# Optimization experiments

Measured on AMD Instinct MI355X. Metric: run time of the kernel, lower is better.

## Reference

```python
import jax, jax.numpy as jnp
import numpy as np

E = 800000   # num edges
N = 50000    # num atoms
C = 128      # in_channels
RBF = 20     # rbf_dim
T = 1        # num_target


def setup_inputs() -> dict:
    key = jax.random.key(0)
    ks = jax.random.split(key, 12)
    return {
        "x_scalar": jax.random.normal(ks[0], (E, C), dtype=jnp.float32),
        "rbf": jax.random.normal(ks[1], (E, RBF), dtype=jnp.float32),
        "envelop_para": jax.random.uniform(ks[2], (E, 1), dtype=jnp.float32),
        "edge_index_0": jax.random.randint(ks[3], (E,), 0, N),
        "num_atoms": N,
        # learned parameters (biases initialized to zero per reset_parameters)
        "W_rbf": jax.random.normal(ks[4], (C, RBF), dtype=jnp.float32) * 0.05,
        "b_rbf": jnp.zeros((C,), dtype=jnp.float32),
        "W1": jax.random.normal(ks[5], (C, C), dtype=jnp.float32) * 0.05,
        "b1": jnp.zeros((C,), dtype=jnp.float32),
        "W2": jax.random.normal(ks[6], (C, C), dtype=jnp.float32) * 0.05,
        "b2": jnp.zeros((C,), dtype=jnp.float32),
        "W3": jax.random.normal(ks[7], (T, C), dtype=jnp.float32) * 0.05,
        "b3": jnp.zeros((T,), dtype=jnp.float32),
    }


def reference(x_scalar, rbf, envelop_para, edge_index_0, num_atoms,
              W_rbf, b_rbf, W1, b1, W2, b2, W3, b3):
    # per-edge filter: Linear(rbf) * envelope, then modulate node features
    rbf_filter = (rbf @ W_rbf.T + b_rbf) * envelop_para  # [E, C]
    msg = rbf_filter * x_scalar                           # [E, C]
    # scatter_add over destination atoms
    out = jax.ops.segment_sum(msg, edge_index_0, num_segments=num_atoms)  # [N, C]
    # small MLP head: Linear+SiLU, Linear+SiLU, Linear -> num_target
    out = jax.nn.silu(out @ W1.T + b1)
    out = jax.nn.silu(out @ W2.T + b2)
    out = out @ W3.T + b3                                 # [N, T]
    return out
```

## Files before the change

### kernel.cpp

```cpp
#include <hip/hip_runtime.h>
#include <hip/hip_bf16.h>

#define C 128
#define RBFD 20
#define NATOMS 50000
#define SCAN_CHUNK 1024
#define SLAB 128
#define SS 32
#define NSS (SLAB / SS)

__global__ __launch_bounds__(256) void setup_kernel(
    const float* __restrict__ W1, const float* __restrict__ W2,
    float* __restrict__ W1T, float* __restrict__ W2T,
    int* __restrict__ count, float4* __restrict__ acc4,
    int n, int acc_quads)
{
    const int t = blockIdx.x * blockDim.x + threadIdx.x;
    const int stride = gridDim.x * blockDim.x;
    if (t < C * C) {
        int k = t / C;
        int c = t % C;
        W1T[t] = W1[c * C + k];
        W2T[t] = W2[c * C + k];
    }
    for (int i = t; i < n; i += stride) count[i] = 0;
    const float4 z = make_float4(0.f, 0.f, 0.f, 0.f);
    for (int i = t; i < acc_quads; i += stride) acc4[i] = z;
}

__global__ __launch_bounds__(256) void histogram_kernel(
    const int* __restrict__ idx, int* __restrict__ count, int E)
{
    int e = blockIdx.x * blockDim.x + threadIdx.x;
    if (e < E) atomicAdd(&count[idx[e]], 1);
}

__global__ __launch_bounds__(256) void scan_partials_kernel(
    const int* __restrict__ count, int* __restrict__ partial, int n)
{
    __shared__ int sm[256];
    const int start = blockIdx.x * SCAN_CHUNK;
    int s = 0;
    for (int i = threadIdx.x; i < SCAN_CHUNK; i += 256) {
        int g = start + i;
        if (g < n) s += count[g];
    }
    sm[threadIdx.x] = s;
    __syncthreads();
    for (int off = 128; off > 0; off >>= 1) {
        if (threadIdx.x < off) sm[threadIdx.x] += sm[threadIdx.x + off];
        __syncthreads();
    }
    if (threadIdx.x == 0) partial[blockIdx.x] = sm[0];
}

__global__ void scan_chunkbase_kernel(int* __restrict__ partial,
                                      int* __restrict__ base,
                                      int nchunks, int n)
{
    if (threadIdx.x == 0 && blockIdx.x == 0) {
        int run = 0;
        for (int k = 0; k < nchunks; ++k) {
            int t = partial[k];
            partial[k] = run;
            run += t;
        }
        base[n] = run;
    }
}

__global__ __launch_bounds__(1024) void scan_apply_kernel(
    const int* __restrict__ count, const int* __restrict__ chunk_base,
    int* __restrict__ base, int* __restrict__ cursor, int n)
{
    __shared__ int sm[SCAN_CHUNK];
    const int t = threadIdx.x;
    const int i = blockIdx.x * SCAN_CHUNK + t;
    int v = (i < n) ? count[i] : 0;
    sm[t] = v;
    __syncthreads();
    for (int off = 1; off < SCAN_CHUNK; off <<= 1) {
        int tmp = (t >= off) ? sm[t - off] : 0;
        __syncthreads();
        sm[t] += tmp;
        __syncthreads();
    }
    if (i < n) {
        int excl = sm[t] - v + chunk_base[blockIdx.x];
        base[i] = excl;
        cursor[i] = excl;
    }
}

__global__ __launch_bounds__(256) void fill_perm_kernel(
    const int* __restrict__ idx, int* __restrict__ cursor,
    int* __restrict__ perm, int* __restrict__ own, int E)
{
    int e = blockIdx.x * blockDim.x + threadIdx.x;
    if (e < E) {
        int a = idx[e];
        int pos = atomicAdd(&cursor[a], 1);
        perm[pos] = e;
        own[pos] = a;
    }
}

__global__ __launch_bounds__(128, 2) void gather_kernel(
    const float* __restrict__ x,
    const float* __restrict__ rbf,
    const float* __restrict__ env,
    const int*   __restrict__ perm,
    const int*   __restrict__ own,
    const float* __restrict__ Wrbf,
    const float* __restrict__ brbf,
    float* __restrict__ acc)
{
    __shared__ int   e_s[SLAB];
    __shared__ float env_s[SLAB];
    __shared__ int   own_s[SLAB];
    __shared__ float rbf_s[2][SS][RBFD];

    const int tid = threadIdx.x;
    const int p0  = blockIdx.x * SLAB;

    {
        const int e = perm[p0 + tid];
        e_s[tid]   = e;
        env_s[tid] = env[e];
        own_s[tid] = own[p0 + tid];
    }

    float w[RBFD];
#pragma unroll
    for (int r = 0; r < RBFD; ++r) w[r] = Wrbf[tid * RBFD + r];
    const float bias = brbf[tid];

    __syncthreads();

    const int first_own = own_s[0];
    int   cur_own = first_own;
    float sum = 0.0f;

#define FLUSH()                                                                \
    do {                                                                       \
        if (cur_own == first_own)                                              \
            unsafeAtomicAdd(&acc[(size_t)cur_own * C + tid], sum);             \
        else acc[(size_t)cur_own * C + tid] = sum;                             \
    } while (0)

    float xr[2][SS];
    float st[5];

#pragma unroll
    for (int p = 0; p < 5; ++p) {
        const int g = p * 128 + tid;
        st[p] = rbf[(size_t)e_s[g / RBFD] * RBFD + (g % RBFD)];
    }
#pragma unroll
    for (int i = 0; i < SS; ++i)
        xr[0][i] = x[(size_t)e_s[i] * C + tid];
    __builtin_amdgcn_sched_barrier(0);
#pragma unroll
    for (int p = 0; p < 5; ++p) {
        const int g = p * 128 + tid;
        rbf_s[0][g / RBFD][g % RBFD] = st[p];
    }
    __syncthreads();

#pragma unroll
    for (int ss = 0; ss < NSS; ++ss) {
        const int sbase = ss * SS;
        const int cur   = ss & 1;

        if (ss + 1 < NSS) {
#pragma unroll
            for (int p = 0; p < 5; ++p) {
                const int g = p * 128 + tid;
                st[p] = rbf[(size_t)e_s[sbase + SS + g / RBFD] * RBFD + (g % RBFD)];
            }
#pragma unroll
            for (int i = 0; i < SS; ++i)
                xr[cur ^ 1][i] = x[(size_t)e_s[sbase + SS + i] * C + tid];
        }
        __builtin_amdgcn_sched_barrier(0);

#pragma unroll
        for (int j = 0; j < SS; ++j) {
            const float4* q = reinterpret_cast<const float4*>(&rbf_s[cur][j][0]);
            const float4 a = q[0], b = q[1], c = q[2], d = q[3], e4 = q[4];
            float f = bias;
            f = fmaf(a.x,  w[0],  f); f = fmaf(a.y,  w[1],  f);
            f = fmaf(a.z,  w[2],  f); f = fmaf(a.w,  w[3],  f);
            f = fmaf(b.x,  w[4],  f); f = fmaf(b.y,  w[5],  f);
            f = fmaf(b.z,  w[6],  f); f = fmaf(b.w,  w[7],  f);
            f = fmaf(c.x,  w[8],  f); f = fmaf(c.y,  w[9],  f);
            f = fmaf(c.z,  w[10], f); f = fmaf(c.w,  w[11], f);
            f = fmaf(d.x,  w[12], f); f = fmaf(d.y,  w[13], f);
            f = fmaf(d.z,  w[14], f); f = fmaf(d.w,  w[15], f);
            f = fmaf(e4.x, w[16], f); f = fmaf(e4.y, w[17], f);
            f = fmaf(e4.z, w[18], f); f = fmaf(e4.w, w[19], f);

            const float v = f * env_s[sbase + j] * xr[cur][j];
            const int   o = own_s[sbase + j];
            if (o != cur_own) { FLUSH(); sum = 0.0f; cur_own = o; }
            sum += v;
        }

        if (ss + 1 < NSS) {
#pragma unroll
            for (int p = 0; p < 5; ++p) {
                const int g = p * 128 + tid;
                rbf_s[cur ^ 1][g / RBFD][g % RBFD] = st[p];
            }
        }
        __syncthreads();
    }
    unsafeAtomicAdd(&acc[(size_t)cur_own * C + tid], sum);
#undef FLUSH
}

__device__ __forceinline__ float silu_f(float v) {
    return v * (1.0f / (1.0f + __expf(-v)));
}

__global__ __launch_bounds__(256) void mlp_head_kernel(
    const float* __restrict__ acc,
    const float* __restrict__ W1T,
    const float* __restrict__ b1,
    const float* __restrict__ W2T,
    const float* __restrict__ b2,
    const float* __restrict__ W3,
    const float* __restrict__ b3,
    float* __restrict__ out,
    int natoms)
{
    __shared__ float As[C][C + 1];

    const int tid = threadIdx.x;
    const int a0  = blockIdx.x * C;
    const int tc  = tid & 15;
    const int ta  = tid >> 4;
    const int abase = ta * 8;
    const int cbase = tc * 8;

    {
        const int sub = tid >> 7;
        const int k   = tid & 127;
        for (int pair = 0; pair < 64; ++pair) {
            const int al = pair * 2 + sub;
            const int a  = a0 + al;
            float v = (a < natoms) ? acc[(size_t)a * C + k] : 0.0f;
            As[k][al] = v;
        }
    }
    __syncthreads();

    float r[8][8];

#pragma unroll
    for (int i = 0; i < 8; ++i)
#pragma unroll
        for (int j = 0; j < 8; ++j) r[i][j] = 0.0f;

#pragma unroll 2
    for (int k = 0; k < C; ++k) {
        float4 bq0 = *reinterpret_cast<const float4*>(W1T + k * C + cbase);
        float4 bq1 = *reinterpret_cast<const float4*>(W1T + k * C + cbase + 4);
        float bv[8] = {bq0.x, bq0.y, bq0.z, bq0.w, bq1.x, bq1.y, bq1.z, bq1.w};
        float av[8];
#pragma unroll
        for (int i = 0; i < 8; ++i) av[i] = As[k][abase + i];
#pragma unroll
        for (int i = 0; i < 8; ++i)
#pragma unroll
            for (int j = 0; j < 8; ++j) r[i][j] = fmaf(av[i], bv[j], r[i][j]);
    }

    __syncthreads();
    {
        float bb[8];
#pragma unroll
        for (int j = 0; j < 8; ++j) bb[j] = b1[cbase + j];
#pragma unroll
        for (int i = 0; i < 8; ++i)
#pragma unroll
            for (int j = 0; j < 8; ++j)
                As[cbase + j][abase + i] = silu_f(r[i][j] + bb[j]);
    }
    __syncthreads();

#pragma unroll
    for (int i = 0; i < 8; ++i)
#pragma unroll
        for (int j = 0; j < 8; ++j) r[i][j] = 0.0f;

#pragma unroll 2
    for (int k = 0; k < C; ++k) {
        float4 bq0 = *reinterpret_cast<const float4*>(W2T + k * C + cbase);
        float4 bq1 = *reinterpret_cast<const float4*>(W2T + k * C + cbase + 4);
        float bv[8] = {bq0.x, bq0.y, bq0.z, bq0.w, bq1.x, bq1.y, bq1.z, bq1.w};
        float av[8];
#pragma unroll
        for (int i = 0; i < 8; ++i) av[i] = As[k][abase + i];
#pragma unroll
        for (int i = 0; i < 8; ++i)
#pragma unroll
            for (int j = 0; j < 8; ++j) r[i][j] = fmaf(av[i], bv[j], r[i][j]);
    }

    __syncthreads();

    {
        float bb[8], w3v[8];
#pragma unroll
        for (int j = 0; j < 8; ++j) bb[j] = b2[cbase + j];
        float4 wq0 = *reinterpret_cast<const float4*>(W3 + cbase);
        float4 wq1 = *reinterpret_cast<const float4*>(W3 + cbase + 4);
        w3v[0]=wq0.x; w3v[1]=wq0.y; w3v[2]=wq0.z; w3v[3]=wq0.w;
        w3v[4]=wq1.x; w3v[5]=wq1.y; w3v[6]=wq1.z; w3v[7]=wq1.w;

#pragma unroll
        for (int i = 0; i < 8; ++i) {
            float p = 0.0f;
#pragma unroll
            for (int j = 0; j < 8; ++j)
                p = fmaf(silu_f(r[i][j] + bb[j]), w3v[j], p);
            As[abase + i][tc] = p;
        }
    }
    __syncthreads();

    if (tid < C) {
        const int a = a0 + tid;
        if (a < natoms) {
            float s = 0.0f;
#pragma unroll
            for (int t = 0; t < 16; ++t) s += As[tid][t];
            out[a] = s + b3[0];
        }
    }
}

extern "C" void kernel_launch(void* const* d_in, const int* in_sizes, int n_in,
                              void* d_out, int out_size, void* d_ws, size_t ws_size,
                              hipStream_t stream) {
    const float* x      = (const float*)d_in[0];
    const float* rbf    = (const float*)d_in[1];
    const float* env    = (const float*)d_in[2];
    const int*   idx    = (const int*)  d_in[3];
    const float* Wrbf   = (const float*)d_in[5];
    const float* brbf   = (const float*)d_in[6];
    const float* W1     = (const float*)d_in[7];
    const float* b1     = (const float*)d_in[8];
    const float* W2     = (const float*)d_in[9];
    const float* b2     = (const float*)d_in[10];
    const float* W3     = (const float*)d_in[11];
    const float* b3     = (const float*)d_in[12];
    float*       out    = (float*)d_out;

    const int E = in_sizes[0] / C;
    const int N = NATOMS;
    const int nchunks = (N + SCAN_CHUNK - 1) / SCAN_CHUNK;

    float* acc     = (float*)d_ws;
    float* W1T     = acc + (size_t)N * C;
    float* W2T     = W1T + C * C;
    int*   count   = (int*)(W2T + C * C);
    int*   base    = count + N;
    int*   cursor  = base + (N + 1);
    int*   partial = cursor + N;
    int*   perm    = partial + 64;
    int*   own     = perm + E;

    setup_kernel<<<2048, 256, 0, stream>>>(W1, W2, W1T, W2T, count,
                                           (float4*)acc, N, (N * C) / 4);

    histogram_kernel<<<(E + 255) / 256, 256, 0, stream>>>(idx, count, E);
    scan_partials_kernel<<<nchunks, 256, 0, stream>>>(count, partial, N);
    scan_chunkbase_kernel<<<1, 64, 0, stream>>>(partial, base, nchunks, N);
    scan_apply_kernel<<<nchunks, SCAN_CHUNK, 0, stream>>>(count, partial, base, cursor, N);
    fill_perm_kernel<<<(E + 255) / 256, 256, 0, stream>>>(idx, cursor, perm, own, E);

    gather_kernel<<<E / SLAB, 128, 0, stream>>>(x, rbf, env, perm, own,
                                                Wrbf, brbf, acc);

    const int tiles = (N + C - 1) / C;
    mlp_head_kernel<<<tiles, 256, 0, stream>>>(acc, W1T, b1, W2T, b2, W3, b3, out, N);
}
```

Before: 330.3 us.

## Hand-pipeline gather loads with inline asm and partial vmcnt waits

Rewrites the gather kernel's slab loop as an explicitly unrolled software pipeline. Global loads are issued through inline asm, and compute runs in 8-edge chunks, each gated by a partial s_waitcnt vmcnt. Compute can then start as soon as the first x rows arrive, rather than waiting for the whole next stage's loads to drain. This trades compiler-managed waits for hand-counted ones, which are fragile if the compiler emits extra memory ops, and raises register pressure from two full x buffers.

```diff
diff --git a/kernel.cpp b/kernel.cpp
--- a/kernel.cpp
+++ b/kernel.cpp
@@ -7,7 +7,6 @@
 #define SCAN_CHUNK 1024
 #define SLAB 128
 #define SS 32
-#define NSS (SLAB / SS)
 
 __global__ __launch_bounds__(256) void setup_kernel(
     const float* __restrict__ W1, const float* __restrict__ W2,
@@ -103,6 +102,28 @@
         perm[pos] = e;
         own[pos] = a;
     }
+}
+
+#define WAITV_(n) asm volatile("s_waitcnt vmcnt(" #n ")" ::: "memory")
+#define WAITV(n)  WAITV_(n)
+
+__device__ __forceinline__ float filt20(const float* __restrict__ row,
+                                        const float* __restrict__ w,
+                                        float bias) {
+    const float4* q = reinterpret_cast<const float4*>(row);
+    const float4 a = q[0], b = q[1], c = q[2], d = q[3], e4 = q[4];
+    float f = bias;
+    f = fmaf(a.x,  w[0],  f); f = fmaf(a.y,  w[1],  f);
+    f = fmaf(a.z,  w[2],  f); f = fmaf(a.w,  w[3],  f);
+    f = fmaf(b.x,  w[4],  f); f = fmaf(b.y,  w[5],  f);
+    f = fmaf(b.z,  w[6],  f); f = fmaf(b.w,  w[7],  f);
+    f = fmaf(c.x,  w[8],  f); f = fmaf(c.y,  w[9],  f);
+    f = fmaf(c.z,  w[10], f); f = fmaf(c.w,  w[11], f);
+    f = fmaf(d.x,  w[12], f); f = fmaf(d.y,  w[13], f);
+    f = fmaf(d.z,  w[14], f); f = fmaf(d.w,  w[15], f);
+    f = fmaf(e4.x, w[16], f); f = fmaf(e4.y, w[17], f);
+    f = fmaf(e4.z, w[18], f); f = fmaf(e4.w, w[19], f);
+    return f;
 }
 
 __global__ __launch_bounds__(128, 2) void gather_kernel(
@@ -137,6 +158,13 @@
 
     __syncthreads();
 
+    asm volatile("" ::
+        "v"(w[0]), "v"(w[1]), "v"(w[2]), "v"(w[3]), "v"(w[4]),
+        "v"(w[5]), "v"(w[6]), "v"(w[7]), "v"(w[8]), "v"(w[9]),
+        "v"(w[10]), "v"(w[11]), "v"(w[12]), "v"(w[13]), "v"(w[14]),
+        "v"(w[15]), "v"(w[16]), "v"(w[17]), "v"(w[18]), "v"(w[19]),
+        "v"(bias));
+
     const int first_own = own_s[0];
     int   cur_own = first_own;
     float sum = 0.0f;
@@ -148,75 +176,101 @@
         else acc[(size_t)cur_own * C + tid] = sum;                             \
     } while (0)
 
-    float xr[2][SS];
-    float st[5];
-
-#pragma unroll
-    for (int p = 0; p < 5; ++p) {
-        const int g = p * 128 + tid;
-        st[p] = rbf[(size_t)e_s[g / RBFD] * RBFD + (g % RBFD)];
-    }
-#pragma unroll
-    for (int i = 0; i < SS; ++i)
-        xr[0][i] = x[(size_t)e_s[i] * C + tid];
+    float xA[SS], xB[SS], st[5];
+
+#define ISSUE_RBF(sb)                                                          \
+    do {                                                                       \
+        _Pragma("unroll")                                                      \
+        for (int p = 0; p < 5; ++p) {                                          \
+            const int g = p * 128 + tid;                                       \
+            const float* ap = rbf + (size_t)e_s[(sb) + g / RBFD] * RBFD        \
+                              + (g % RBFD);                                    \
+            asm volatile("global_load_dword %0, %1, off"                       \
+                         : "=v"(st[p]) : "v"(ap));                             \
+        }                                                                      \
+    } while (0)
+
+#define ISSUE_X(sb, XB)                                                        \
+    do {                                                                       \
+        _Pragma("unroll")                                                      \
+        for (int i = 0; i < SS; ++i) {                                         \
+            const float* ap = x + ((size_t)e_s[(sb) + i] << 7) + tid;          \
+            asm volatile("global_load_dword %0, %1, off"                       \
+                         : "=v"(XB[i]) : "v"(ap));                             \
+        }                                                                      \
+    } while (0)
+
+#define CHUNK8(sb, j0, XB, B, WN)                                              \
+    do {                                                                       \
+        WAITV(WN);                                                             \
+        __builtin_amdgcn_sched_barrier(0);                                     \
+        _Pragma("unroll")                                                      \
+        for (int j = (j0); j < (j0) + 8; ++j) {                                \
+            const float f = filt20(&rbf_s[B][j][0], w, bias);                  \
+            const float v = f * env_s[(sb) + j] * XB[j];                       \
+            const int   o = own_s[(sb) + j];                                   \
+            if (o != cur_own) { FLUSH(); sum = 0.0f; cur_own = o; }            \
+            sum += v;                                                          \
+        }                                                                      \
+    } while (0)
+
+#define STAGE_DSWRITE(B)                                                       \
+    do {                                                                       \
+        WAITV(32);                                                             \
+        __builtin_amdgcn_sched_barrier(0);                                     \
+        _Pragma("unroll")                                                      \
+        for (int p = 0; p < 5; ++p) {                                          \
+            const int g = p * 128 + tid;                                       \
+            rbf_s[B][g / RBFD][g % RBFD] = st[p];                              \
+        }                                                                      \
+        asm volatile("s_waitcnt lgkmcnt(0)" ::: "memory");                     \
+        __builtin_amdgcn_sched_barrier(0);                                     \
+        __builtin_amdgcn_s_barrier();                                          \
+    } while (0)
+
+    ISSUE_RBF(0);
+    ISSUE_X(0, xA);
+    STAGE_DSWRITE(0);
+
+    ISSUE_RBF(SS);
+    ISSUE_X(SS, xB);
     __builtin_amdgcn_sched_barrier(0);
-#pragma unroll
-    for (int p = 0; p < 5; ++p) {
-        const int g = p * 128 + tid;
-        rbf_s[0][g / RBFD][g % RBFD] = st[p];
-    }
-    __syncthreads();
-
-#pragma unroll
-    for (int ss = 0; ss < NSS; ++ss) {
-        const int sbase = ss * SS;
-        const int cur   = ss & 1;
-
-        if (ss + 1 < NSS) {
-#pragma unroll
-            for (int p = 0; p < 5; ++p) {
-                const int g = p * 128 + tid;
-                st[p] = rbf[(size_t)e_s[sbase + SS + g / RBFD] * RBFD + (g % RBFD)];
-            }
-#pragma unroll
-            for (int i = 0; i < SS; ++i)
-                xr[cur ^ 1][i] = x[(size_t)e_s[sbase + SS + i] * C + tid];
-        }
-        __builtin_amdgcn_sched_barrier(0);
-
-#pragma unroll
-        for (int j = 0; j < SS; ++j) {
-            const float4* q = reinterpret_cast<const float4*>(&rbf_s[cur][j][0]);
-            const float4 a = q[0], b = q[1], c = q[2], d = q[3], e4 = q[4];
-            float f = bias;
-            f = fmaf(a.x,  w[0],  f); f = fmaf(a.y,  w[1],  f);
-            f = fmaf(a.z,  w[2],  f); f = fmaf(a.w,  w[3],  f);
-            f = fmaf(b.x,  w[4],  f); f = fmaf(b.y,  w[5],  f);
-            f = fmaf(b.z,  w[6],  f); f = fmaf(b.w,  w[7],  f);
-            f = fmaf(c.x,  w[8],  f); f = fmaf(c.y,  w[9],  f);
-            f = fmaf(c.z,  w[10], f); f = fmaf(c.w,  w[11], f);
-            f = fmaf(d.x,  w[12], f); f = fmaf(d.y,  w[13], f);
-            f = fmaf(d.z,  w[14], f); f = fmaf(d.w,  w[15], f);
-            f = fmaf(e4.x, w[16], f); f = fmaf(e4.y, w[17], f);
-            f = fmaf(e4.z, w[18], f); f = fmaf(e4.w, w[19], f);
-
-            const float v = f * env_s[sbase + j] * xr[cur][j];
-            const int   o = own_s[sbase + j];
-            if (o != cur_own) { FLUSH(); sum = 0.0f; cur_own = o; }
-            sum += v;
-        }
-
-        if (ss + 1 < NSS) {
-#pragma unroll
-            for (int p = 0; p < 5; ++p) {
-                const int g = p * 128 + tid;
-                rbf_s[cur ^ 1][g / RBFD][g % RBFD] = st[p];
-            }
-        }
-        __syncthreads();
-    }
+    CHUNK8(0, 0,  xA, 0, 61);
+    CHUNK8(0, 8,  xA, 0, 53);
+    CHUNK8(0, 16, xA, 0, 45);
+    CHUNK8(0, 24, xA, 0, 37);
+    STAGE_DSWRITE(1);
+
+    ISSUE_RBF(2 * SS);
+    ISSUE_X(2 * SS, xA);
+    __builtin_amdgcn_sched_barrier(0);
+    CHUNK8(SS, 0,  xB, 1, 61);
+    CHUNK8(SS, 8,  xB, 1, 53);
+    CHUNK8(SS, 16, xB, 1, 45);
+    CHUNK8(SS, 24, xB, 1, 37);
+    STAGE_DSWRITE(0);
+
+    ISSUE_RBF(3 * SS);
+    ISSUE_X(3 * SS, xB);
+    __builtin_amdgcn_sched_barrier(0);
+    CHUNK8(2 * SS, 0,  xA, 0, 61);
+    CHUNK8(2 * SS, 8,  xA, 0, 53);
+    CHUNK8(2 * SS, 16, xA, 0, 45);
+    CHUNK8(2 * SS, 24, xA, 0, 37);
+    STAGE_DSWRITE(1);
+
+    CHUNK8(3 * SS, 0,  xB, 1, 24);
+    CHUNK8(3 * SS, 8,  xB, 1, 16);
+    CHUNK8(3 * SS, 16, xB, 1, 8);
+    CHUNK8(3 * SS, 24, xB, 1, 0);
+
     unsafeAtomicAdd(&acc[(size_t)cur_own * C + tid], sum);
+
 #undef FLUSH
+#undef ISSUE_RBF
+#undef ISSUE_X
+#undef CHUNK8
+#undef STAGE_DSWRITE
 }
 
 __device__ __forceinline__ float silu_f(float v) {
```

New measurement: 346.1 us. 1.05x slower.
